# Optimization experiments

Measured on AMD Instinct MI355X. Metric: run time of the kernel, lower is better.

The kernel has to match this reference:

```python
import jax, jax.numpy as jnp
import numpy as np
from jax import lax

NUM_CLASSES = 80
RADIUS = 2.5
TOPK = 10
IOU_W = 3.0
CLS_W = 1.0
A = 33600
G = 256
IMG = 640.0


def setup_inputs() -> dict:
    key = jax.random.key(0)
    k1, k2, k3, k4, k5, k6, k7 = jax.random.split(key, 7)

    def _boxes(kc, kw, n):
        c = jax.random.uniform(kc, (n, 2), jnp.float32, 0.0, IMG)
        wh = jax.random.uniform(kw, (n, 2), jnp.float32, 8.0, 128.0)
        return jnp.concatenate([c - wh / 2, c + wh / 2], axis=1)

    return {
        "pred_scores": jax.random.normal(k1, (A, NUM_CLASSES), jnp.float32),
        "pred_bboxes": _boxes(k2, k3, A),
        "anchor_points": jax.random.uniform(k6, (A, 2), jnp.float32, 0.0, IMG),
        "gt_labels": jax.random.randint(k7, (G,), 0, NUM_CLASSES),
        "gt_bboxes": _boxes(k4, k5, G),
    }


def _inside_flags(anchor_points, gt_bboxes):
    # [G, A] bool: anchor inside GT box AND inside center-sampling region
    ax = anchor_points[None, :, 0]  # [1, A]
    ay = anchor_points[None, :, 1]
    x1, y1, x2, y2 = (gt_bboxes[:, i:i + 1] for i in range(4))  # each [G, 1]
    in_gt = (ax >= x1) & (ax <= x2) & (ay >= y1) & (ay <= y2)
    cx, cy = (x1 + x2) / 2, (y1 + y2) / 2
    rx, ry = RADIUS * (x2 - x1), RADIUS * (y2 - y1)
    in_center = (ax >= cx - rx) & (ax <= cx + rx) & (ay >= cy - ry) & (ay <= cy + ry)
    return in_gt & in_center


def _pairwise_iou(gt_bboxes, pred_bboxes, eps=1e-6):
    # [G, A]
    lt = jnp.maximum(gt_bboxes[:, None, :2], pred_bboxes[None, :, :2])
    rb = jnp.minimum(gt_bboxes[:, None, 2:], pred_bboxes[None, :, 2:])
    wh = jnp.clip(rb - lt, 0.0)
    overlap = wh[..., 0] * wh[..., 1]
    area_g = (gt_bboxes[:, 2] - gt_bboxes[:, 0]) * (gt_bboxes[:, 3] - gt_bboxes[:, 1])
    area_p = (pred_bboxes[:, 2] - pred_bboxes[:, 0]) * (pred_bboxes[:, 3] - pred_bboxes[:, 1])
    union = area_g[:, None] + area_p[None, :] - overlap + eps
    return overlap / union


def _simota(pred_scores, pred_bboxes, anchor_points, gt_labels, gt_bboxes):
    num_gt = gt_bboxes.shape[0]
    num_anchors = pred_scores.shape[0]
    gt_labels = gt_labels.astype(jnp.int32)

    inside = _inside_flags(anchor_points, gt_bboxes)  # [G, A] bool
    ious = _pairwise_iou(gt_bboxes, pred_bboxes)      # [G, A]

    # BCE(sigmoid(s), one_hot(l)) summed over classes, without [G, A, C]:
    # cost[g,a] = -sum_c log(1-p[a,c]) - (log p[a,l_g] - log(1-p[a,l_g]))
    logp = jax.nn.log_sigmoid(pred_scores)       # [A, C] = log p
    log1mp = jax.nn.log_sigmoid(-pred_scores)    # [A, C] = log(1-p)
    cls_cost = -(logp - log1mp)[:, gt_labels].T - log1mp.sum(-1)[None, :]  # [G, A]

    iou_cost = -jnp.log(ious)
    cost = CLS_W * cls_cost + IOU_W * iou_cost + (~inside).astype(cost_dtype := jnp.float32) * 1e10
    cost = lax.stop_gradient(cost)  # cost only feeds integer top-k indices

    num_candidates = ((ious * inside.astype(ious.dtype)) > 0).sum(axis=1)
    dynamic_ks = jnp.clip(num_candidates, 1, TOPK)  # [G]

    # fixed top-TOPK smallest cost per GT, mask to dynamic_k
    _, topk_idx = lax.top_k(-cost, TOPK)  # [G, TOPK]
    valid = jnp.arange(TOPK)[None, :] < dynamic_ks[:, None]
    idx = jnp.where(valid, topk_idx, num_anchors)  # invalid -> sentinel slot
    g_ids = jnp.broadcast_to(jnp.arange(num_gt, dtype=jnp.int32)[:, None], (num_gt, TOPK))
    # sequential overwrite by ascending gt index == per-anchor max gt index
    assigned = (jnp.full((num_anchors + 1,), -1, jnp.int32)
                .at[idx.reshape(-1)].max(g_ids.reshape(-1)))[:num_anchors]

    pos = assigned >= 0
    safe_g = jnp.where(pos, assigned, 0)
    assigned_labels = jnp.where(pos, gt_labels[safe_g], NUM_CLASSES)
    assigned_bboxes = jnp.where(pos[:, None], gt_bboxes[safe_g], 0.0)
    pos_iou = ious[safe_g, jnp.arange(num_anchors)]
    assigned_scores = (jnp.zeros((num_anchors, NUM_CLASSES + 1), ious.dtype)
                       .at[jnp.arange(num_anchors), assigned_labels]
                       .set(jnp.where(pos, pos_iou, 0.0)))
    return assigned_labels, assigned_bboxes, assigned_scores


def reference(pred_scores, pred_bboxes, anchor_points, gt_labels, gt_bboxes):
    return _simota(pred_scores, pred_bboxes, anchor_points, gt_labels, gt_bboxes)
```

## Files before the change

### kernel.cpp

```cpp
#include <hip/hip_runtime.h>
#include <climits>

#define A_N 33600
#define G_N 256
#define NC 80
#define KK 10
#define CAP 2048
#define GCHUNK 32
#define NCHUNK (G_N / GCHUNK)
#define NLD 32
#define FILL_N ((A_N * 81) / 4)

__device__ __forceinline__ unsigned int ford(float f) {
    unsigned int u = __float_as_uint(f);
    return (u & 0x80000000u) ? ~u : (u | 0x80000000u);
}

__device__ __forceinline__ unsigned long long umin64(unsigned long long a, unsigned long long b) {
    return a < b ? a : b;
}

__global__ __launch_bounds__(256) void k_init(
    const float* __restrict__ scores, float* __restrict__ logsum,
    int* __restrict__ cnt, int* __restrict__ assigned,
    float* __restrict__ out_labels, float4* __restrict__ out_bbox4,
    float4* __restrict__ out_scores4)
{
    int t = blockIdx.x * 256 + threadIdx.x;
    int wv = t >> 6, lane = t & 63;
    float4 z4 = make_float4(0.f, 0.f, 0.f, 0.f);

    if (t < G_N) cnt[t] = 0;
    if (t < A_N) { assigned[t] = -1; out_labels[t] = (float)NC; out_bbox4[t] = z4; }
    if (t < FILL_N) out_scores4[t] = z4;

    const float* row = scores + (long)wv * NC;
    float acc = 0.f;
    for (int c = lane; c < NC; c += 64) {
        float s = row[c];
        acc -= (fmaxf(s, 0.f) + log1pf(expf(-fabsf(s))));
    }
    #pragma unroll
    for (int off = 32; off > 0; off >>= 1) acc += __shfl_down(acc, off);
    if (lane == 0) logsum[wv] = acc;
}

__global__ __launch_bounds__(256) void k_pairs(
    const float* __restrict__ scores, const float* __restrict__ pred_b,
    const float* __restrict__ anchors, const int* __restrict__ gt_labels,
    const float* __restrict__ gt_b, const float* __restrict__ logsum,
    unsigned long long* __restrict__ bucket, int* __restrict__ cnt)
{
    __shared__ float4 gbox[GCHUNK];
    __shared__ int glab[GCHUNK];
    int tid = threadIdx.x;
    int gc = blockIdx.y;
    if (tid < GCHUNK) {
        gbox[tid] = ((const float4*)gt_b)[gc * GCHUNK + tid];
        glab[tid] = gt_labels[gc * GCHUNK + tid];
    }
    __syncthreads();

    int a = blockIdx.x * 256 + tid;
    if (a >= A_N) return;

    float4 pb = ((const float4*)pred_b)[a];
    float2 ap = ((const float2*)anchors)[a];
    float area_p = (pb.z - pb.x) * (pb.w - pb.y);
    float ls = logsum[a];

    #pragma unroll 4
    for (int g = 0; g < GCHUNK; g++) {
        float4 gb = gbox[g];
        bool in_gt = (ap.x >= gb.x) & (ap.x <= gb.z) & (ap.y >= gb.y) & (ap.y <= gb.w);
        if (!in_gt) continue;

        float ltx = fmaxf(gb.x, pb.x), lty = fmaxf(gb.y, pb.y);
        float rbx = fminf(gb.z, pb.z), rby = fminf(gb.w, pb.w);
        float w = fmaxf(rbx - ltx, 0.f), h = fmaxf(rby - lty, 0.f);
        float overlap = w * h;
        if (!(overlap > 0.f)) continue;

        int gg = gc * GCHUNK + g;
        float area_g = (gb.z - gb.x) * (gb.w - gb.y);
        float uni = area_g + area_p - overlap + 1e-6f;
        float iou = overlap / uni;
        float s = scores[(long)a * NC + glab[g]];
        float cost = (-s - ls) + 3.0f * (-logf(iou));
        unsigned long long key = ((unsigned long long)ford(cost) << 32) | (unsigned)a;

        int slot = atomicAdd(&cnt[gg], 1);
        if ((unsigned)slot < CAP) bucket[(size_t)gg * CAP + slot] = key;
    }
}

__global__ __launch_bounds__(64) void k_select(
    const unsigned long long* __restrict__ bucket, const int* __restrict__ cnt_arr,
    const float* __restrict__ pred_b, const float* __restrict__ gt_b,
    int* __restrict__ assigned, int* __restrict__ poslist)
{
    int g = blockIdx.x, lane = threadIdx.x;
    int cnt = cnt_arr[g];

    if (cnt == 0) {
        float4 gb = ((const float4*)gt_b)[g];
        int found = INT_MAX;
        for (int base = 0; base < A_N; base += 64) {
            int a = base + lane;
            float4 pb = ((const float4*)pred_b)[a];
            float w = fminf(gb.z, pb.z) - fmaxf(gb.x, pb.x);
            float h = fminf(gb.w, pb.w) - fmaxf(gb.y, pb.y);
            bool hit = (w > 0.f) && (h > 0.f);
            if (__ballot(hit)) { if (hit) found = a; break; }
        }
        #pragma unroll
        for (int off = 32; off; off >>= 1) found = min(found, __shfl_xor(found, off));
        int m = (found == INT_MAX) ? 0 : found;
        if (lane == 0) atomicMax(&assigned[m], g);
        if (lane < KK) poslist[g * KK + lane] = (lane == 0) ? m : -1;
        return;
    }

    int k = cnt < KK ? cnt : KK;
    int nreal = cnt < CAP ? cnt : CAP;
    const unsigned long long* bk = bucket + (size_t)g * CAP;

    unsigned long long kv[NLD];
    #pragma unroll
    for (int i = 0; i < NLD; i++) {
        kv[i] = ~0ull;
        if (i * 64 < nreal) {
            int idx = lane + i * 64;
            if (idx < nreal) kv[i] = bk[idx];
        }
    }

    int mywin = -1;
    for (int it = 0; it < k; it++) {
        unsigned long long m = ~0ull;
        #pragma unroll
        for (int i = 0; i < NLD; i++) if (i * 64 < nreal) m = umin64(m, kv[i]);
        #pragma unroll
        for (int off = 32; off; off >>= 1) m = umin64(m, __shfl_xor(m, off));
        if (lane == it) mywin = (int)(m & 0xffffffffu);
        #pragma unroll
        for (int i = 0; i < NLD; i++) if (i * 64 < nreal) { if (kv[i] == m) kv[i] = ~0ull; }
    }

    if (lane < KK) poslist[g * KK + lane] = (lane < k) ? mywin : -1;
    if (lane < k) atomicMax(&assigned[mywin], g);
}

__global__ __launch_bounds__(256) void k_fix(
    const int* __restrict__ poslist, const int* __restrict__ assigned,
    const int* __restrict__ gt_labels, const float* __restrict__ gt_b,
    const float* __restrict__ pred_b,
    float* __restrict__ out_labels, float4* __restrict__ out_bbox4,
    float* __restrict__ out_scores)
{
    int t = blockIdx.x * 256 + threadIdx.x;
    if (t >= G_N * KK) return;
    int a = poslist[t];
    if (a < 0) return;
    int g = assigned[a];
    int label = gt_labels[g];
    float4 gb = ((const float4*)gt_b)[g];
    float4 pb = ((const float4*)pred_b)[a];
    float w = fminf(gb.z, pb.z) - fmaxf(gb.x, pb.x);
    float h = fminf(gb.w, pb.w) - fmaxf(gb.y, pb.y);
    float ovl = fmaxf(w, 0.f) * fmaxf(h, 0.f);
    float area_g = (gb.z - gb.x) * (gb.w - gb.y);
    float area_p = (pb.z - pb.x) * (pb.w - pb.y);
    float uni = area_g + area_p - ovl + 1e-6f;
    float iou = ovl / uni;
    out_labels[a] = (float)label;
    out_bbox4[a] = gb;
    out_scores[(long)a * (NC + 1) + label] = iou;
}

extern "C" void kernel_launch(void* const* d_in, const int* in_sizes, int n_in,
                              void* d_out, int out_size, void* d_ws, size_t ws_size,
                              hipStream_t stream) {
    const float* pred_scores   = (const float*)d_in[0];
    const float* pred_bboxes   = (const float*)d_in[1];
    const float* anchor_points = (const float*)d_in[2];
    const int*   gt_labels     = (const int*)d_in[3];
    const float* gt_bboxes     = (const float*)d_in[4];

    char* ws = (char*)d_ws;
    unsigned long long* bucket = (unsigned long long*)ws;
    size_t off = (size_t)G_N * CAP * 8;
    int*   assigned = (int*)(ws + off);   off += (size_t)A_N * 4;
    int*   cnt      = (int*)(ws + off);   off += (size_t)G_N * 4;
    int*   poslist  = (int*)(ws + off);   off += (size_t)G_N * KK * 4;
    float* logsum   = (float*)(ws + off);

    float*  out_labels = (float*)d_out;
    float4* out_bbox4  = (float4*)(out_labels + A_N);
    float*  out_scores = out_labels + 5 * (size_t)A_N;

    k_init<<<A_N / 4, 256, 0, stream>>>(pred_scores, logsum, cnt, assigned,
                                        out_labels, out_bbox4, (float4*)out_scores);
    dim3 pg((A_N + 255) / 256, NCHUNK);
    k_pairs<<<pg, 256, 0, stream>>>(pred_scores, pred_bboxes, anchor_points,
                                    gt_labels, gt_bboxes, logsum, bucket, cnt);
    k_select<<<G_N, 64, 0, stream>>>(bucket, cnt, pred_bboxes, gt_bboxes,
                                     assigned, poslist);
    k_fix<<<(G_N * KK + 255) / 256, 256, 0, stream>>>(poslist, assigned, gt_labels,
                                                      gt_bboxes, pred_bboxes,
                                                      out_labels, out_bbox4, out_scores);
}
```

Baseline: 45.79 us.

## Replace atomic candidate buckets with bitmask candidates and per-lane top-k select

The pair kernel now writes a per-GT bitmask of anchors that lie inside the box and overlap it, built with wave ballots, instead of appending cost keys to buckets through atomics. It is fused with the init/logsum kernel into a single launch. The select kernel walks the set bits, computes IoU and cost only for those candidates, and keeps a per-lane sorted top-10 list, which removes the 2048-entry bucket loads and the cap. In exchange, cost computation moves into the 256-block select kernel, whose work per GT is serialized over set bits and depends on load balance.

```diff
diff --git a/kernel.cpp b/kernel.cpp
--- a/kernel.cpp
+++ b/kernel.cpp
@@ -5,10 +5,12 @@
 #define G_N 256
 #define NC 80
 #define KK 10
-#define CAP 2048
 #define GCHUNK 32
 #define NCHUNK (G_N / GCHUNK)
-#define NLD 32
+#define AB_N 132
+#define PAIR_BLKS (AB_N * NCHUNK)
+#define INIT_BLKS (A_N / 4)
+#define NW (AB_N * 4)
 #define FILL_N ((A_N * 81) / 4)
 
 __device__ __forceinline__ unsigned int ford(float f) {
@@ -20,20 +22,54 @@
     return a < b ? a : b;
 }
 
-__global__ __launch_bounds__(256) void k_init(
-    const float* __restrict__ scores, float* __restrict__ logsum,
-    int* __restrict__ cnt, int* __restrict__ assigned,
+__global__ __launch_bounds__(256) void k_phase1(
+    const float* __restrict__ scores, const float* __restrict__ pred_b,
+    const float* __restrict__ anchors, const float* __restrict__ gt_b,
+    unsigned long long* __restrict__ mask, float* __restrict__ logsum,
+    int* __restrict__ assigned,
     float* __restrict__ out_labels, float4* __restrict__ out_bbox4,
     float4* __restrict__ out_scores4)
 {
-    int t = blockIdx.x * 256 + threadIdx.x;
-    int wv = t >> 6, lane = t & 63;
+    int bid = blockIdx.x, tid = threadIdx.x;
+    int lane = tid & 63, wid = tid >> 6;
+
+    if (bid < PAIR_BLKS) {
+        __shared__ float4 gbox[GCHUNK];
+        int gc = bid & (NCHUNK - 1);
+        int ab = bid >> 3;
+        if (tid < GCHUNK) gbox[tid] = ((const float4*)gt_b)[gc * GCHUNK + tid];
+        __syncthreads();
+
+        int a = ab * 256 + tid;
+        bool valid = a < A_N;
+        int as = valid ? a : (A_N - 1);
+        float4 pb = ((const float4*)pred_b)[as];
+        float2 ap = ((const float2*)anchors)[as];
+        int word = ab * 4 + wid;
+
+        #pragma unroll 4
+        for (int g = 0; g < GCHUNK; g++) {
+            float4 gb = gbox[g];
+            bool in_gt = valid &&
+                (ap.x >= gb.x) && (ap.x <= gb.z) && (ap.y >= gb.y) && (ap.y <= gb.w);
+            unsigned long long em = 0;
+            if (__ballot(in_gt)) {
+                float ltx = fmaxf(gb.x, pb.x), lty = fmaxf(gb.y, pb.y);
+                float rbx = fminf(gb.z, pb.z), rby = fminf(gb.w, pb.w);
+                float w = fmaxf(rbx - ltx, 0.f), h = fmaxf(rby - lty, 0.f);
+                em = __ballot(in_gt && (w * h > 0.f));
+            }
+            if (lane == 0) mask[(size_t)(gc * GCHUNK + g) * NW + word] = em;
+        }
+        return;
+    }
+
+    int t = (bid - PAIR_BLKS) * 256 + tid;
     float4 z4 = make_float4(0.f, 0.f, 0.f, 0.f);
-
-    if (t < G_N) cnt[t] = 0;
     if (t < A_N) { assigned[t] = -1; out_labels[t] = (float)NC; out_bbox4[t] = z4; }
     if (t < FILL_N) out_scores4[t] = z4;
 
+    int wv = t >> 6;
     const float* row = scores + (long)wv * NC;
     float acc = 0.f;
     for (int c = lane; c < NC; c += 64) {
@@ -45,71 +81,35 @@
     if (lane == 0) logsum[wv] = acc;
 }
 
-__global__ __launch_bounds__(256) void k_pairs(
-    const float* __restrict__ scores, const float* __restrict__ pred_b,
-    const float* __restrict__ anchors, const int* __restrict__ gt_labels,
-    const float* __restrict__ gt_b, const float* __restrict__ logsum,
-    unsigned long long* __restrict__ bucket, int* __restrict__ cnt)
-{
-    __shared__ float4 gbox[GCHUNK];
-    __shared__ int glab[GCHUNK];
-    int tid = threadIdx.x;
-    int gc = blockIdx.y;
-    if (tid < GCHUNK) {
-        gbox[tid] = ((const float4*)gt_b)[gc * GCHUNK + tid];
-        glab[tid] = gt_labels[gc * GCHUNK + tid];
-    }
-    __syncthreads();
-
-    int a = blockIdx.x * 256 + tid;
-    if (a >= A_N) return;
-
-    float4 pb = ((const float4*)pred_b)[a];
-    float2 ap = ((const float2*)anchors)[a];
-    float area_p = (pb.z - pb.x) * (pb.w - pb.y);
-    float ls = logsum[a];
-
-    #pragma unroll 4
-    for (int g = 0; g < GCHUNK; g++) {
-        float4 gb = gbox[g];
-        bool in_gt = (ap.x >= gb.x) & (ap.x <= gb.z) & (ap.y >= gb.y) & (ap.y <= gb.w);
-        if (!in_gt) continue;
-
-        float ltx = fmaxf(gb.x, pb.x), lty = fmaxf(gb.y, pb.y);
-        float rbx = fminf(gb.z, pb.z), rby = fminf(gb.w, pb.w);
-        float w = fmaxf(rbx - ltx, 0.f), h = fmaxf(rby - lty, 0.f);
-        float overlap = w * h;
-        if (!(overlap > 0.f)) continue;
-
-        int gg = gc * GCHUNK + g;
-        float area_g = (gb.z - gb.x) * (gb.w - gb.y);
-        float uni = area_g + area_p - overlap + 1e-6f;
-        float iou = overlap / uni;
-        float s = scores[(long)a * NC + glab[g]];
-        float cost = (-s - ls) + 3.0f * (-logf(iou));
-        unsigned long long key = ((unsigned long long)ford(cost) << 32) | (unsigned)a;
-
-        int slot = atomicAdd(&cnt[gg], 1);
-        if ((unsigned)slot < CAP) bucket[(size_t)gg * CAP + slot] = key;
-    }
-}
-
 __global__ __launch_bounds__(64) void k_select(
-    const unsigned long long* __restrict__ bucket, const int* __restrict__ cnt_arr,
-    const float* __restrict__ pred_b, const float* __restrict__ gt_b,
+    const unsigned long long* __restrict__ mask, const float* __restrict__ scores,
+    const float* __restrict__ logsum, const float* __restrict__ pred_b,
+    const float* __restrict__ gt_b, const int* __restrict__ gt_labels,
     int* __restrict__ assigned, int* __restrict__ poslist)
 {
     int g = blockIdx.x, lane = threadIdx.x;
-    int cnt = cnt_arr[g];
+    const unsigned long long* mr = mask + (size_t)g * NW;
+
+    unsigned long long wbuf[9];
+    int cnt = 0;
+    #pragma unroll
+    for (int i = 0; i < 9; i++) {
+        int idx = i * 64 + lane;
+        wbuf[i] = (idx < NW) ? mr[idx] : 0ull;
+        cnt += __popcll(wbuf[i]);
+    }
+    #pragma unroll
+    for (int off = 32; off; off >>= 1) cnt += __shfl_xor(cnt, off);
+
+    float4 gb = ((const float4*)gt_b)[g];
 
     if (cnt == 0) {
-        float4 gb = ((const float4*)gt_b)[g];
         int found = INT_MAX;
         for (int base = 0; base < A_N; base += 64) {
             int a = base + lane;
-            float4 pb = ((const float4*)pred_b)[a];
-            float w = fminf(gb.z, pb.z) - fmaxf(gb.x, pb.x);
-            float h = fminf(gb.w, pb.w) - fmaxf(gb.y, pb.y);
+            float4 pbx = ((const float4*)pred_b)[a];
+            float w = fminf(gb.z, pbx.z) - fmaxf(gb.x, pbx.x);
+            float h = fminf(gb.w, pbx.w) - fmaxf(gb.y, pbx.y);
             bool hit = (w > 0.f) && (h > 0.f);
             if (__ballot(hit)) { if (hit) found = a; break; }
         }
@@ -121,30 +121,57 @@
         return;
     }
 
+    int lg = gt_labels[g];
+    float area_g = (gb.z - gb.x) * (gb.w - gb.y);
+
+    unsigned long long p[KK];
+    #pragma unroll
+    for (int i = 0; i < KK; i++) p[i] = ~0ull;
+
+    #pragma unroll
+    for (int i = 0; i < 9; i++) {
+        unsigned long long bits = wbuf[i];
+        int abase = (i * 64 + lane) * 64;
+        while (bits) {
+            int b = __builtin_ctzll(bits);
+            bits &= bits - 1;
+            int a = abase + b;
+            float4 pbx = ((const float4*)pred_b)[a];
+            float ltx = fmaxf(gb.x, pbx.x), lty = fmaxf(gb.y, pbx.y);
+            float rbx = fminf(gb.z, pbx.z), rby = fminf(gb.w, pbx.w);
+            float w = fmaxf(rbx - ltx, 0.f), h = fmaxf(rby - lty, 0.f);
+            float overlap = w * h;
+            float area_p = (pbx.z - pbx.x) * (pbx.w - pbx.y);
+            float uni = area_g + area_p - overlap + 1e-6f;
+            float iou = overlap / uni;
+            float s = scores[(long)a * NC + lg];
+            float cost = (-s - logsum[a]) + 3.0f * (-logf(iou));
+            unsigned long long key = ((unsigned long long)ford(cost) << 32) | (unsigned)a;
+            if (key < p[KK - 1]) {
+                p[KK - 1] = key;
+                #pragma unroll
+                for (int k2 = KK - 1; k2 > 0; k2--) {
+                    unsigned long long lo = p[k2-1] < p[k2] ? p[k2-1] : p[k2];
+                    unsigned long long hi = p[k2-1] < p[k2] ? p[k2]   : p[k2-1];
+                    p[k2-1] = lo; p[k2] = hi;
+                }
+            }
+        }
+    }
+
     int k = cnt < KK ? cnt : KK;
-    int nreal = cnt < CAP ? cnt : CAP;
-    const unsigned long long* bk = bucket + (size_t)g * CAP;
-
-    unsigned long long kv[NLD];
-    #pragma unroll
-    for (int i = 0; i < NLD; i++) {
-        kv[i] = ~0ull;
-        if (i * 64 < nreal) {
-            int idx = lane + i * 64;
-            if (idx < nreal) kv[i] = bk[idx];
-        }
-    }
-
     int mywin = -1;
     for (int it = 0; it < k; it++) {
-        unsigned long long m = ~0ull;
-        #pragma unroll
-        for (int i = 0; i < NLD; i++) if (i * 64 < nreal) m = umin64(m, kv[i]);
+        unsigned long long m = p[0];
         #pragma unroll
         for (int off = 32; off; off >>= 1) m = umin64(m, __shfl_xor(m, off));
         if (lane == it) mywin = (int)(m & 0xffffffffu);
-        #pragma unroll
-        for (int i = 0; i < NLD; i++) if (i * 64 < nreal) { if (kv[i] == m) kv[i] = ~0ull; }
+        bool win = (p[0] == m);
+        if (win) {
+            #pragma unroll
+            for (int k2 = 0; k2 < KK - 1; k2++) p[k2] = p[k2 + 1];
+            p[KK - 1] = ~0ull;
+        }
     }
 
     if (lane < KK) poslist[g * KK + lane] = (lane < k) ? mywin : -1;
@@ -188,10 +215,9 @@
     const float* gt_bboxes     = (const float*)d_in[4];
 
     char* ws = (char*)d_ws;
-    unsigned long long* bucket = (unsigned long long*)ws;
-    size_t off = (size_t)G_N * CAP * 8;
+    unsigned long long* mask = (unsigned long long*)ws;
+    size_t off = (size_t)G_N * NW * 8;
     int*   assigned = (int*)(ws + off);   off += (size_t)A_N * 4;
-    int*   cnt      = (int*)(ws + off);   off += (size_t)G_N * 4;
     int*   poslist  = (int*)(ws + off);   off += (size_t)G_N * KK * 4;
     float* logsum   = (float*)(ws + off);
 
@@ -199,13 +225,11 @@
     float4* out_bbox4  = (float4*)(out_labels + A_N);
     float*  out_scores = out_labels + 5 * (size_t)A_N;
 
-    k_init<<<A_N / 4, 256, 0, stream>>>(pred_scores, logsum, cnt, assigned,
-                                        out_labels, out_bbox4, (float4*)out_scores);
-    dim3 pg((A_N + 255) / 256, NCHUNK);
-    k_pairs<<<pg, 256, 0, stream>>>(pred_scores, pred_bboxes, anchor_points,
-                                    gt_labels, gt_bboxes, logsum, bucket, cnt);
-    k_select<<<G_N, 64, 0, stream>>>(bucket, cnt, pred_bboxes, gt_bboxes,
-                                     assigned, poslist);
+    k_phase1<<<PAIR_BLKS + INIT_BLKS, 256, 0, stream>>>(
+        pred_scores, pred_bboxes, anchor_points, gt_bboxes,
+        mask, logsum, assigned, out_labels, out_bbox4, (float4*)out_scores);
+    k_select<<<G_N, 64, 0, stream>>>(mask, pred_scores, logsum, pred_bboxes,
+                                     gt_bboxes, gt_labels, assigned, poslist);
     k_fix<<<(G_N * KK + 255) / 256, 256, 0, stream>>>(poslist, assigned, gt_labels,
                                                       gt_bboxes, pred_bboxes,
                                                       out_labels, out_bbox4, out_scores);
```

Result: faster. 43.92 us (-4.1%).
